# Kernel tuning notes

Measured on AMD Instinct MI355X. Metric: run time of the kernel, lower is better.

The kernel has to match this reference:

```python
import jax, jax.numpy as jnp
import numpy as np

N_FEATURES = 170
D_MODEL = 64
N_HEADS = 4
ALPHA = 0.1
LN_EPS = 1e-5
LEAKY_SLOPE = 0.01  # torch F.leaky_relu default
N = 3 * N_FEATURES  # 510
B = 32


def setup_inputs() -> dict:
    key = jax.random.key(0)
    ks = jax.random.split(key, 10)
    D, H = D_MODEL, N_HEADS
    s = 1.0 / np.sqrt(D)
    return {
        "x": jax.random.normal(ks[0], (B, N, D), dtype=jnp.float32),
        "causal_graph": jax.random.uniform(ks[1], (N, N), dtype=jnp.float32),
        # nn.Linear(d_model, d_model*n_heads, bias=False): stored here as (D, H*D) for x @ W
        "W": jax.random.uniform(ks[2], (D, H * D), jnp.float32, -s, s),
        "attention_w": jax.random.normal(ks[3], (H, 2 * D), dtype=jnp.float32),
        # Conv2d(2, n_heads, 3, padding=1): OIHW kernel
        "conv_w": jax.random.uniform(ks[4], (H, 2, 3, 3), jnp.float32, -1/np.sqrt(18), 1/np.sqrt(18)),
        "conv_b": jax.random.uniform(ks[5], (H,), jnp.float32, -1/np.sqrt(18), 1/np.sqrt(18)),
        # nn.Linear(d_model, 2*d_model): stored as (D, 2D)
        "fcg_w": jax.random.uniform(ks[6], (D, 2 * D), jnp.float32, -s, s),
        "fcg_b": jax.random.uniform(ks[7], (2 * D,), jnp.float32, -s, s),
        "ln_g": jnp.ones((D,), jnp.float32),
        "ln_b": jnp.zeros((D,), jnp.float32),
    }


def reference(x, causal_graph, W, attention_w, conv_w, conv_b, fcg_w, fcg_b, ln_g, ln_b):
    Bz, Nn, D = x.shape
    H = N_HEADS
    # shared projection: (B, N, H, D)
    xt = (x @ W).reshape(Bz, Nn, H, D)
    # GAT-style additive scores: concat-dot decomposed into two dot products
    w1, w2 = attention_w[:, :D], attention_w[:, D:]  # each (H, D)
    s_i = jnp.einsum('bnhd,hd->bhn', xt, w1)  # source term
    s_j = jnp.einsum('bnhd,hd->bhn', xt, w2)  # target term
    e = s_i[:, :, :, None] + s_j[:, :, None, :]  # (B, H, N, N)
    A_eva = jnp.where(e >= 0, e, LEAKY_SLOPE * e)  # leaky_relu
    # fuse mean attention with causal graph via 3x3 conv
    A_mean = A_eva.mean(axis=1)  # (B, N, N)
    causal = jnp.broadcast_to(causal_graph[None], (Bz, Nn, Nn))
    stacked = jnp.stack([A_mean, causal], axis=1)  # (B, 2, N, N)
    A_st = jax.lax.conv_general_dilated(
        stacked, conv_w, window_strides=(1, 1), padding=((1, 1), (1, 1)),
        dimension_numbers=('NCHW', 'OIHW', 'NCHW'))
    A_st = A_st + conv_b[None, :, None, None]  # (B, H, N, N)
    A = jax.nn.softmax(ALPHA * A_eva + (1.0 - ALPHA) * A_st, axis=-1)
    # multi-head aggregation then head-mean
    out = jnp.einsum('bhnm,bmhd->bnhd', A, xt).mean(axis=2)  # (B, N, D)
    # GLU
    g = out @ fcg_w + fcg_b  # (B, N, 2D)
    a, b = g[..., :D], g[..., D:]
    glu = a * jax.nn.sigmoid(b)
    # residual + layernorm
    y = glu + x
    mu = y.mean(axis=-1, keepdims=True)
    var = ((y - mu) ** 2).mean(axis=-1, keepdims=True)
    y = (y - mu) * jax.lax.rsqrt(var + LN_EPS) * ln_g + ln_b
    return y, A
```

## Files before the change

kernel.cpp:

```cpp
#include <hip/hip_runtime.h>

#define Bz 32
#define Nn 510
#define Dd 64
#define Hh 4
#define HD_ 256
#define Kpad 512
#define ALPHA_ 0.1f
#define LNEPS 1e-5f
#define SLOPE 0.01f
#define NEG_INF -3.0e38f

typedef __attribute__((ext_vector_type(8))) short short8;
typedef __attribute__((ext_vector_type(4))) float floatx4;

__device__ inline float wredsum(float v) {
  #pragma unroll
  for (int off = 32; off; off >>= 1) v += __shfl_xor(v, off, 64);
  return v;
}
__device__ inline float wredmax(float v) {
  #pragma unroll
  for (int off = 32; off; off >>= 1) v = fmaxf(v, __shfl_xor(v, off, 64));
  return v;
}
__device__ inline unsigned short f2bf(float f) {
  unsigned int u = __float_as_uint(f);
  unsigned int r = (u + 0x7fffu + ((u >> 16) & 1u)) >> 16;
  return (unsigned short)r;
}

__global__ __launch_bounds__(256) void k1_xt(const float* __restrict__ x,
                                             const float* __restrict__ W,
                                             const float* __restrict__ attw,
                                             unsigned short* __restrict__ xtT,
                                             float* __restrict__ si,
                                             float* __restrict__ sj) {
  __shared__ float Wl[64][132];
  __shared__ float xr[32][68];
  __shared__ unsigned short st[128 * 65];
  const int t = threadIdx.x;
  const int rt = blockIdx.x;
  const int b = blockIdx.y;
  const int ch = blockIdx.z;
  #pragma unroll
  for (int k = 0; k < 8; k++) {
    int f = t + k * 256;
    int kr = f >> 5;
    int c = (f & 31) * 4;
    float4 v = *(const float4*)&W[kr * HD_ + ch * 128 + c];
    *(float4*)&Wl[kr][c] = v;
  }
  #pragma unroll
  for (int k = 0; k < 2; k++) {
    int f = t + k * 256;
    int r = f >> 4;
    int c = (f & 15) * 4;
    int row = rt * 32 + r;
    float4 v = make_float4(0.f, 0.f, 0.f, 0.f);
    if (row < Nn) v = *(const float4*)&x[(b * Nn + row) * Dd + c];
    *(float4*)&xr[r][c] = v;
  }
  __syncthreads();
  const int tr = t >> 5, tc = t & 31;
  const int rb = tr * 4, c0 = tc * 4;
  float acc[4][4] = {};
  #pragma unroll
  for (int k4 = 0; k4 < 16; k4++) {
    float4 xv[4];
    #pragma unroll
    for (int r = 0; r < 4; r++) xv[r] = *(float4*)&xr[rb + r][k4 * 4];
    #pragma unroll
    for (int kk = 0; kk < 4; kk++) {
      float4 wv = *(float4*)&Wl[k4 * 4 + kk][c0];
      #pragma unroll
      for (int r = 0; r < 4; r++) {
        float xs = (&xv[r].x)[kk];
        acc[r][0] = fmaf(xs, wv.x, acc[r][0]);
        acc[r][1] = fmaf(xs, wv.y, acc[r][1]);
        acc[r][2] = fmaf(xs, wv.z, acc[r][2]);
        acc[r][3] = fmaf(xs, wv.w, acc[r][3]);
      }
    }
  }
  #pragma unroll
  for (int cc = 0; cc < 4; cc++) {
    #pragma unroll
    for (int r = 0; r < 4; r++) {
      st[(c0 + cc) * 65 + rb + r] = f2bf(acc[r][cc]);
    }
  }
  const int colbase = ch * 128 + c0;
  const int h = colbase >> 6;
  const int dd = colbase & 63;
  const int m0r = rt * 32 + rb;
  float w1v[4], w2v[4];
  #pragma unroll
  for (int cc = 0; cc < 4; cc++) {
    w1v[cc] = attw[h * 128 + dd + cc];
    w2v[cc] = attw[h * 128 + 64 + dd + cc];
  }
  #pragma unroll
  for (int r = 0; r < 4; r++) {
    float p1 = acc[r][0] * w1v[0] + acc[r][1] * w1v[1] +
               acc[r][2] * w1v[2] + acc[r][3] * w1v[3];
    float p2 = acc[r][0] * w2v[0] + acc[r][1] * w2v[1] +
               acc[r][2] * w2v[2] + acc[r][3] * w2v[3];
    #pragma unroll
    for (int off = 1; off <= 8; off <<= 1) {
      p1 += __shfl_xor(p1, off, 64);
      p2 += __shfl_xor(p2, off, 64);
    }
    if ((tc & 15) == 0) {
      int row = m0r + r;
      if (row < Nn) {
        si[(b * 4 + h) * Nn + row] = p1;
        sj[(b * 4 + h) * Nn + row] = p2;
      }
    }
  }
  __syncthreads();
  {
    const int rowd = t >> 1;
    const int part = t & 1;
    const int colb2 = ch * 128 + rowd;
    const int h2 = colb2 >> 6;
    const int dd2 = colb2 & 63;
    unsigned short* dst =
        &xtT[((size_t)(b * 4 + h2) * 64 + dd2) * Kpad + rt * 32 + part * 16];
    short8 v0, v1;
    #pragma unroll
    for (int k = 0; k < 8; k++) {
      v0[k] = (short)st[rowd * 65 + part * 16 + k];
      v1[k] = (short)st[rowd * 65 + part * 16 + 8 + k];
    }
    *(short8*)&dst[0] = v0;
    *(short8*)&dst[8] = v1;
  }
}

__global__ __launch_bounds__(256) void k2_attn(const float* __restrict__ si,
                                               const float* __restrict__ sj,
                                               const float* __restrict__ causal,
                                               const float* __restrict__ convw,
                                               const float* __restrict__ convb,
                                               float* __restrict__ A) {
  __shared__ float am_t[10 * 8 * 68];
  __shared__ float cz_t[10 * 8 * 68];
  __shared__ float sjl[4 * 8 * 68];
  __shared__ float sil[4][12];
  const int t = threadIdx.x;
  const int i0 = blockIdx.x * 8;
  const int b = blockIdx.y;
  if (t < 40) {
    int h = t / 10, r = t % 10;
    int iq = i0 + r - 1;
    sil[h][r] = (iq >= 0 && iq < Nn) ? si[(b * 4 + h) * Nn + iq] : 0.f;
  }
  if (t >= 64 && t < 224) {
    int q = t - 64;
    int r = q >> 4, rem = q & 15;
    int e = rem >> 1, side = rem & 1;
    int idx = (r * 8 + e) * 68 + side * 65;
    am_t[idx] = 0.f;
    cz_t[idx] = 0.f;
  }
  for (int f = t; f < 2048; f += 256) {
    int h = f >> 9, j = f & 511;
    float v = (j < Nn) ? sj[(b * 4 + h) * Nn + j] : 0.f;
    sjl[(h * 8 + (j & 7)) * 68 + (j >> 3) + 1] = v;
  }
  __syncthreads();
  for (int f = t; f < 5120; f += 256) {
    int r = f >> 9, j = f & 511;
    int iq = i0 + r - 1;
    float am = 0.f, cz = 0.f;
    if (iq >= 0 && iq < Nn && j < Nn) {
      float s = 0.f;
      #pragma unroll
      for (int h = 0; h < 4; h++) {
        float e2 = sil[h][r] + sjl[(h * 8 + (j & 7)) * 68 + (j >> 3) + 1];
        s += (e2 >= 0.f) ? e2 : SLOPE * e2;
      }
      am = 0.25f * s;
      cz = causal[iq * Nn + j];
    }
    int idx = (r * 8 + (j & 7)) * 68 + (j >> 3) + 1;
    am_t[idx] = am;
    cz_t[idx] = cz;
  }
  __syncthreads();
  const int w = t >> 6, L = t & 63;
  const int j0 = L * 8;
  for (int pp = w; pp < 32; pp += 4) {
    const int il = pp >> 2, h = pp & 3;
    const int i = i0 + il;
    if (i >= Nn) continue;
    const int bh = b * 4 + h;
    const float sih = sil[h][il + 1];
    float cw[18];
    #pragma unroll
    for (int q = 0; q < 18; q++) cw[q] = convw[h * 18 + q];
    const float cb = convb[h];
    float conv[8];
    #pragma unroll
    for (int e = 0; e < 8; e++) conv[e] = cb;
    #pragma unroll
    for (int r3 = 0; r3 < 3; r3++) {
      const float* ba = &am_t[((il + r3) * 8) * 68];
      const float* bc = &cz_t[((il + r3) * 8) * 68];
      float a[10], c[10];
      a[0] = ba[7 * 68 + L];
      c[0] = bc[7 * 68 + L];
      #pragma unroll
      for (int e = 0; e < 8; e++) {
        a[1 + e] = ba[e * 68 + L + 1];
        c[1 + e] = bc[e * 68 + L + 1];
      }
      a[9] = ba[0 * 68 + L + 2];
      c[9] = bc[0 * 68 + L + 2];
      float w0 = cw[r3 * 3], w1 = cw[r3 * 3 + 1], w2 = cw[r3 * 3 + 2];
      float u0 = cw[9 + r3 * 3], u1 = cw[9 + r3 * 3 + 1], u2 = cw[9 + r3 * 3 + 2];
      #pragma unroll
      for (int e = 0; e < 8; e++) {
        float cv = conv[e];
        cv = fmaf(w0, a[e], cv);
        cv = fmaf(w1, a[e + 1], cv);
        cv = fmaf(w2, a[e + 2], cv);
        cv = fmaf(u0, c[e], cv);
        cv = fmaf(u1, c[e + 1], cv);
        cv = fmaf(u2, c[e + 2], cv);
        conv[e] = cv;
      }
    }
    float v[8];
    float mx = NEG_INF;
    #pragma unroll
    for (int e = 0; e < 8; e++) {
      float ee = sih + sjl[(h * 8 + e) * 68 + L + 1];
      float l = (ee >= 0.f) ? ee : SLOPE * ee;
      float val = ALPHA_ * l + (1.0f - ALPHA_) * conv[e];
      v[e] = (j0 + e < Nn) ? val : NEG_INF;
      mx = fmaxf(mx, v[e]);
    }
    mx = wredmax(mx);
    float p[8], s = 0.f;
    #pragma unroll
    for (int e = 0; e < 8; e++) {
      p[e] = __expf(v[e] - mx);
      s += p[e];
    }
    s = wredsum(s);
    const float inv = 1.f / s;
    #pragma unroll
    for (int e = 0; e < 8; e++) p[e] *= inv;
    float* Ar = &A[((size_t)bh * Nn + i) * Nn + j0];
    *(float4*)&Ar[0] = make_float4(p[0], p[1], p[2], p[3]);
    if (L < 63) {
      *(float4*)&Ar[4] = make_float4(p[4], p[5], p[6], p[7]);
    } else {
      *(float2*)&Ar[4] = make_float2(p[4], p[5]);
    }
  }
}

__global__ __launch_bounds__(256) void k3_out(const float* __restrict__ A,
                                              const unsigned short* __restrict__ xtT,
                                              const float* __restrict__ x,
                                              const float* __restrict__ fcgw,
                                              const float* __restrict__ fcgb,
                                              const float* __restrict__ lng,
                                              const float* __restrict__ lnb,
                                              float* __restrict__ y) {
  __shared__ unsigned short Asub[16 * 72];
  __shared__ unsigned short Xsub[64 * 72];
  __shared__ float ol[16][64];
  __shared__ float gl[2][128];
  const int t = threadIdx.x;
  const int n0 = blockIdx.x * 16;
  const int b = blockIdx.y;
  const int w = t >> 6, lane = t & 63;
  const int quad = lane >> 4, l16 = lane & 15;
  const int wc = w * 16;
  const int ar = t >> 4;
  const int amc = (t & 15) * 4;
  const int xd = t >> 2;
  const int xmc = (t & 3) * 16;
  floatx4 acc = {0.f, 0.f, 0.f, 0.f};
  for (int h = 0; h < 4; h++) {
    const float* Ab = &A[((size_t)(b * 4 + h) * Nn + n0) * Nn];
    const unsigned short* Xb = &xtT[(size_t)(b * 4 + h) * 64 * Kpad];
    for (int kt = 0; kt < 8; kt++) {
      const int m0 = kt * 64;
      __syncthreads();
      {
        int n = n0 + ar;
        int m = m0 + amc;
        float av[4] = {0.f, 0.f, 0.f, 0.f};
        if (n < Nn) {
          const float* src = &Ab[(size_t)ar * Nn + m];
          if (m + 3 < Nn) {
            *(float4*)av = *(const float4*)src;
          } else {
            int lim = Nn - m;
            #pragma unroll
            for (int q = 0; q < 4; q++) if (q < lim) av[q] = src[q];
          }
        }
        ushort4 u;
        u.x = f2bf(av[0]); u.y = f2bf(av[1]);
        u.z = f2bf(av[2]); u.w = f2bf(av[3]);
        *(ushort4*)&Asub[ar * 72 + amc] = u;
        const unsigned short* xs = &Xb[(size_t)xd * Kpad + m0 + xmc];
        short8 x0 = *(const short8*)&xs[0];
        short8 x1 = *(const short8*)&xs[8];
        *(short8*)&Xsub[xd * 72 + xmc] = x0;
        *(short8*)&Xsub[xd * 72 + xmc + 8] = x1;
      }
      __syncthreads();
      #pragma unroll
      for (int ks = 0; ks < 2; ks++) {
        short8 af = *(short8*)&Asub[l16 * 72 + ks * 32 + quad * 8];
        short8 bf = *(short8*)&Xsub[(wc + l16) * 72 + ks * 32 + quad * 8];
        acc = __builtin_amdgcn_mfma_f32_16x16x32_bf16(af, bf, acc, 0, 0, 0);
      }
    }
  }
  __syncthreads();
  #pragma unroll
  for (int reg = 0; reg < 4; reg++) {
    ol[quad * 4 + reg][wc + l16] = 0.25f * acc[reg];
  }
  __syncthreads();
  const int kk = t & 127;
  const int rg = t >> 7;
  for (int it = 0; it < 8; it++) {
    const int r = it * 2 + rg;
    const int row = n0 + r;
    float g = fcgb[kk];
    #pragma unroll
    for (int d = 0; d < 64; d++) g = fmaf(ol[r][d], fcgw[d * 128 + kk], g);
    gl[rg][kk] = g;
    __syncthreads();
    if (kk < 64 && row < Nn) {
      float a = gl[rg][kk];
      float bb = gl[rg][kk + 64];
      float glu = a / (1.f + __expf(-bb));
      float yv = glu + x[(b * Nn + row) * Dd + kk];
      float mu = wredsum(yv) * (1.f / 64.f);
      float dv = yv - mu;
      float var = wredsum(dv * dv) * (1.f / 64.f);
      float o = dv * rsqrtf(var + LNEPS) * lng[kk] + lnb[kk];
      y[(b * Nn + row) * Dd + kk] = o;
    }
    __syncthreads();
  }
}

extern "C" void kernel_launch(void* const* d_in, const int* in_sizes, int n_in,
                              void* d_out, int out_size, void* d_ws, size_t ws_size,
                              hipStream_t stream) {
  const float* x      = (const float*)d_in[0];
  const float* causal = (const float*)d_in[1];
  const float* W      = (const float*)d_in[2];
  const float* attw   = (const float*)d_in[3];
  const float* convw  = (const float*)d_in[4];
  const float* convb  = (const float*)d_in[5];
  const float* fcgw   = (const float*)d_in[6];
  const float* fcgb   = (const float*)d_in[7];
  const float* lng    = (const float*)d_in[8];
  const float* lnb    = (const float*)d_in[9];

  float* ws = (float*)d_ws;
  float* si = ws;
  float* sj = si + (size_t)Bz * Hh * Nn;
  unsigned short* xtT = (unsigned short*)(sj + (size_t)Bz * Hh * Nn + 16);

  float* yout = (float*)d_out;
  float* Aout = yout + (size_t)Bz * Nn * Dd;

  k1_xt <<<dim3(16, Bz, 2), 256, 0, stream>>>(x, W, attw, xtT, si, sj);
  k2_attn<<<dim3(64, Bz), 256, 0, stream>>>(si, sj, causal, convw, convb, Aout);
  k3_out <<<dim3(32, Bz), 256, 0, stream>>>(Aout, xtT, x, fcgw, fcgb, lng, lnb, yout);
}
```

Measured before the change: 277.5 us.

## Fuse attention softmax with aggregation, GLU and layernorm in one kernel

Merges the attention kernel and the output kernel. Each block keeps its 8 rows of softmax probabilities for all heads in shared memory as bf16 and runs the MFMA aggregation, GLU and layernorm directly, so A is no longer re-read from global memory. A is still written out because it is a required output. The cost is that half of each 16-row MFMA tile is padding, and each block re-reads xtT for only 8 rows, which doubles total xtT traffic. The heavier per-block work may also lower occupancy.

```diff
diff --git a/kernel.cpp b/kernel.cpp
--- a/kernel.cpp
+++ b/kernel.cpp
@@ -139,16 +139,25 @@
   }
 }
 
-__global__ __launch_bounds__(256) void k2_attn(const float* __restrict__ si,
-                                               const float* __restrict__ sj,
-                                               const float* __restrict__ causal,
-                                               const float* __restrict__ convw,
-                                               const float* __restrict__ convb,
-                                               float* __restrict__ A) {
-  __shared__ float am_t[10 * 8 * 68];
-  __shared__ float cz_t[10 * 8 * 68];
+#define PST 2064
+__global__ __launch_bounds__(256) void k2_fused(const float* __restrict__ si,
+                                                const float* __restrict__ sj,
+                                                const float* __restrict__ causal,
+                                                const float* __restrict__ convw,
+                                                const float* __restrict__ convb,
+                                                const unsigned short* __restrict__ xtT,
+                                                const float* __restrict__ x,
+                                                const float* __restrict__ fcgw,
+                                                const float* __restrict__ fcgb,
+                                                const float* __restrict__ lng,
+                                                const float* __restrict__ lnb,
+                                                float* __restrict__ A,
+                                                float* __restrict__ y) {
+  __shared__ __align__(16) float smem[10880];
   __shared__ float sjl[4 * 8 * 68];
   __shared__ float sil[4][12];
+  float* am_t = smem;
+  float* cz_t = smem + 5440;
   const int t = threadIdx.x;
   const int i0 = blockIdx.x * 8;
   const int b = blockIdx.y;
@@ -192,16 +201,17 @@
   __syncthreads();
   const int w = t >> 6, L = t & 63;
   const int j0 = L * 8;
-  for (int pp = w; pp < 32; pp += 4) {
-    const int il = pp >> 2, h = pp & 3;
+  const int h = w;
+  const int bh = b * 4 + h;
+  float cw[18];
+  #pragma unroll
+  for (int q = 0; q < 18; q++) cw[q] = convw[h * 18 + q];
+  const float cb = convb[h];
+  unsigned int pr[8][4];
+  #pragma unroll
+  for (int il = 0; il < 8; il++) {
     const int i = i0 + il;
-    if (i >= Nn) continue;
-    const int bh = b * 4 + h;
     const float sih = sil[h][il + 1];
-    float cw[18];
-    #pragma unroll
-    for (int q = 0; q < 18; q++) cw[q] = convw[h * 18 + q];
-    const float cb = convb[h];
     float conv[8];
     #pragma unroll
     for (int e = 0; e < 8; e++) conv[e] = cb;
@@ -254,97 +264,66 @@
     const float inv = 1.f / s;
     #pragma unroll
     for (int e = 0; e < 8; e++) p[e] *= inv;
-    float* Ar = &A[((size_t)bh * Nn + i) * Nn + j0];
-    *(float4*)&Ar[0] = make_float4(p[0], p[1], p[2], p[3]);
-    if (L < 63) {
-      *(float4*)&Ar[4] = make_float4(p[4], p[5], p[6], p[7]);
-    } else {
-      *(float2*)&Ar[4] = make_float2(p[4], p[5]);
-    }
-  }
-}
-
-__global__ __launch_bounds__(256) void k3_out(const float* __restrict__ A,
-                                              const unsigned short* __restrict__ xtT,
-                                              const float* __restrict__ x,
-                                              const float* __restrict__ fcgw,
-                                              const float* __restrict__ fcgb,
-                                              const float* __restrict__ lng,
-                                              const float* __restrict__ lnb,
-                                              float* __restrict__ y) {
-  __shared__ unsigned short Asub[16 * 72];
-  __shared__ unsigned short Xsub[64 * 72];
-  __shared__ float ol[16][64];
-  __shared__ float gl[2][128];
-  const int t = threadIdx.x;
-  const int n0 = blockIdx.x * 16;
-  const int b = blockIdx.y;
-  const int w = t >> 6, lane = t & 63;
-  const int quad = lane >> 4, l16 = lane & 15;
+    #pragma unroll
+    for (int q = 0; q < 4; q++) {
+      pr[il][q] = ((unsigned int)f2bf(p[2 * q + 1]) << 16) | f2bf(p[2 * q]);
+    }
+    if (i < Nn) {
+      float* Ar = &A[((size_t)bh * Nn + i) * Nn + j0];
+      *(float4*)&Ar[0] = make_float4(p[0], p[1], p[2], p[3]);
+      if (L < 63) {
+        *(float4*)&Ar[4] = make_float4(p[4], p[5], p[6], p[7]);
+      } else {
+        *(float2*)&Ar[4] = make_float2(p[4], p[5]);
+      }
+    }
+  }
+  __syncthreads();
+  unsigned short* P = (unsigned short*)smem;
+  #pragma unroll
+  for (int il = 0; il < 8; il++) {
+    *(uint4*)&P[(size_t)il * PST + h * 512 + j0] =
+        make_uint4(pr[il][0], pr[il][1], pr[il][2], pr[il][3]);
+  }
+  __syncthreads();
+  const int quad = L >> 4, l16 = L & 15;
   const int wc = w * 16;
-  const int ar = t >> 4;
-  const int amc = (t & 15) * 4;
-  const int xd = t >> 2;
-  const int xmc = (t & 3) * 16;
   floatx4 acc = {0.f, 0.f, 0.f, 0.f};
-  for (int h = 0; h < 4; h++) {
-    const float* Ab = &A[((size_t)(b * 4 + h) * Nn + n0) * Nn];
-    const unsigned short* Xb = &xtT[(size_t)(b * 4 + h) * 64 * Kpad];
-    for (int kt = 0; kt < 8; kt++) {
-      const int m0 = kt * 64;
-      __syncthreads();
-      {
-        int n = n0 + ar;
-        int m = m0 + amc;
-        float av[4] = {0.f, 0.f, 0.f, 0.f};
-        if (n < Nn) {
-          const float* src = &Ab[(size_t)ar * Nn + m];
-          if (m + 3 < Nn) {
-            *(float4*)av = *(const float4*)src;
-          } else {
-            int lim = Nn - m;
-            #pragma unroll
-            for (int q = 0; q < 4; q++) if (q < lim) av[q] = src[q];
-          }
-        }
-        ushort4 u;
-        u.x = f2bf(av[0]); u.y = f2bf(av[1]);
-        u.z = f2bf(av[2]); u.w = f2bf(av[3]);
-        *(ushort4*)&Asub[ar * 72 + amc] = u;
-        const unsigned short* xs = &Xb[(size_t)xd * Kpad + m0 + xmc];
-        short8 x0 = *(const short8*)&xs[0];
-        short8 x1 = *(const short8*)&xs[8];
-        *(short8*)&Xsub[xd * 72 + xmc] = x0;
-        *(short8*)&Xsub[xd * 72 + xmc + 8] = x1;
-      }
-      __syncthreads();
-      #pragma unroll
-      for (int ks = 0; ks < 2; ks++) {
-        short8 af = *(short8*)&Asub[l16 * 72 + ks * 32 + quad * 8];
-        short8 bf = *(short8*)&Xsub[(wc + l16) * 72 + ks * 32 + quad * 8];
-        acc = __builtin_amdgcn_mfma_f32_16x16x32_bf16(af, bf, acc, 0, 0, 0);
-      }
-    }
-  }
-  __syncthreads();
+  #pragma unroll
+  for (int h2 = 0; h2 < 4; h2++) {
+    const unsigned short* Xh =
+        &xtT[((size_t)(b * 4 + h2) * 64 + (wc + l16)) * Kpad];
+    #pragma unroll 4
+    for (int kt = 0; kt < 16; kt++) {
+      short8 af = {0, 0, 0, 0, 0, 0, 0, 0};
+      if (l16 < 8)
+        af = *(const short8*)&P[l16 * PST + h2 * 512 + kt * 32 + quad * 8];
+      short8 bf = *(const short8*)&Xh[kt * 32 + quad * 8];
+      acc = __builtin_amdgcn_mfma_f32_16x16x32_bf16(af, bf, acc, 0, 0, 0);
+    }
+  }
+  __syncthreads();
+  float* ol = smem + 8256;
+  float* gl = smem + 8768;
   #pragma unroll
   for (int reg = 0; reg < 4; reg++) {
-    ol[quad * 4 + reg][wc + l16] = 0.25f * acc[reg];
+    int row = quad * 4 + reg;
+    if (row < 8) ol[row * 64 + wc + l16] = 0.25f * acc[reg];
   }
   __syncthreads();
   const int kk = t & 127;
   const int rg = t >> 7;
-  for (int it = 0; it < 8; it++) {
+  for (int it = 0; it < 4; it++) {
     const int r = it * 2 + rg;
-    const int row = n0 + r;
+    const int row = i0 + r;
     float g = fcgb[kk];
     #pragma unroll
-    for (int d = 0; d < 64; d++) g = fmaf(ol[r][d], fcgw[d * 128 + kk], g);
-    gl[rg][kk] = g;
+    for (int d = 0; d < 64; d++) g = fmaf(ol[r * 64 + d], fcgw[d * 128 + kk], g);
+    gl[rg * 128 + kk] = g;
     __syncthreads();
     if (kk < 64 && row < Nn) {
-      float a = gl[rg][kk];
-      float bb = gl[rg][kk + 64];
+      float a = gl[rg * 128 + kk];
+      float bb = gl[rg * 128 + kk + 64];
       float glu = a / (1.f + __expf(-bb));
       float yv = glu + x[(b * Nn + row) * Dd + kk];
       float mu = wredsum(yv) * (1.f / 64.f);
@@ -379,7 +358,8 @@
   float* yout = (float*)d_out;
   float* Aout = yout + (size_t)Bz * Nn * Dd;
 
-  k1_xt <<<dim3(16, Bz, 2), 256, 0, stream>>>(x, W, attw, xtT, si, sj);
-  k2_attn<<<dim3(64, Bz), 256, 0, stream>>>(si, sj, causal, convw, convb, Aout);
-  k3_out <<<dim3(32, Bz), 256, 0, stream>>>(Aout, xtT, x, fcgw, fcgb, lng, lnb, yout);
-}
+  k1_xt   <<<dim3(16, Bz, 2), 256, 0, stream>>>(x, W, attw, xtT, si, sj);
+  k2_fused<<<dim3(64, Bz), 256, 0, stream>>>(si, sj, causal, convw, convb,
+                                             xtT, x, fcgw, fcgb, lng, lnb,
+                                             Aout, yout);
+}
```

Result: slower. 417.9 us (+50.6%).
